# Performance work log

Measured on AMD Instinct MI355X. Metric: run time of the kernel, lower is better.

The kernel has to match this reference:

```python
import jax, jax.numpy as jnp
import numpy as np

N_NODES = 50000


def _sage_conv(x, src, dst, W_l, b_l, W_r):
    # PyG SAGEConv (aggr='mean'): out = lin_l(mean_{j in N(i)} x_j) + lin_r(x_i)
    # lin_l has bias, lin_r has no bias.
    neigh_sum = jax.ops.segment_sum(x[src], dst, num_segments=N_NODES)  # [N, F]
    deg = jax.ops.segment_sum(jnp.ones_like(dst, dtype=x.dtype), dst, num_segments=N_NODES)
    neigh_mean = neigh_sum / jnp.maximum(deg, 1.0)[:, None]
    return neigh_mean @ W_l.T + b_l + x @ W_r.T


def setup_inputs() -> dict:
    key = jax.random.key(0)
    ks = jax.random.split(key, 8)
    D, H, C = 768, 128, 4
    x = jax.random.normal(ks[0], (N_NODES, D), dtype=jnp.float32)
    edge_index = jax.random.randint(ks[1], (2, 800000), 0, N_NODES, dtype=jnp.int64)
    s1 = 1.0 / np.sqrt(D)
    s2 = 1.0 / np.sqrt(H)
    return {
        "x": x,
        "edge_index": edge_index,
        "W1_l": jax.random.uniform(ks[2], (H, D), jnp.float32, -s1, s1),
        "b1_l": jnp.zeros((H,), jnp.float32),
        "W1_r": jax.random.uniform(ks[3], (H, D), jnp.float32, -s1, s1),
        "W2_l": jax.random.uniform(ks[4], (C, H), jnp.float32, -s2, s2),
        "b2_l": jnp.zeros((C,), jnp.float32),
        "W2_r": jax.random.uniform(ks[5], (C, H), jnp.float32, -s2, s2),
    }


def reference(x, edge_index, W1_l, b1_l, W1_r, W2_l, b2_l, W2_r):
    src, dst = edge_index[0], edge_index[1]
    h = jax.nn.relu(_sage_conv(x, src, dst, W1_l, b1_l, W1_r))  # [N, H]
    out = _sage_conv(h, src, dst, W2_l, b2_l, W2_r)  # [N, C]
    return out
```

## Files before the change

### kernel.cpp

```cpp
#include <hip/hip_runtime.h>


typedef __bf16 bf16x8 __attribute__((ext_vector_type(8)));
typedef float  f32x4  __attribute__((ext_vector_type(4)));

__device__ __forceinline__ float bf16_lo(uint32_t w) {
    union { uint32_t u; float f; } c; c.u = w << 16; return c.f;
}
__device__ __forceinline__ float bf16_hi(uint32_t w) {
    union { uint32_t u; float f; } c; c.u = w & 0xffff0000u; return c.f;
}

__global__ __launch_bounds__(256)
void prep(const float* __restrict__ W1l, const float* __restrict__ W1r,
          __bf16* __restrict__ Bp, int* __restrict__ deg, int N)
{
    int i = blockIdx.x * 256 + threadIdx.x;
    if (i < N) deg[i] = 0;
    if (i < 256 * 768) {
        int col = i / 768, k = i - col * 768;
        float v = (col < 128) ? W1l[col * 768 + k] : W1r[(col - 128) * 768 + k];
        Bp[((k >> 3) << 11) + (col << 3) + (k & 7)] = (__bf16)v;
    }
}

__global__ __launch_bounds__(512)
void gemm_bf16(const float* __restrict__ A, const __bf16* __restrict__ Bp,
               __bf16* __restrict__ Cb, int M)
{
    constexpr int LDK = 72;
    __shared__ __bf16 As[64][LDK];
    const int bm   = blockIdx.x * 64;
    const int tid  = threadIdx.x;
    const int lane = tid & 63;
    const int wave = tid >> 6;
    const int wr = wave >> 2, wc = wave & 3;
    const int l15 = lane & 15;
    const int lk  = lane >> 4;

    f32x4 acc[2][4] = {};
    float4 apref[2];

    const int arow = tid >> 3;
    const int akc  = (tid & 7) << 3;
    const __bf16* bbase = Bp + ((size_t)(wc * 64 + l15) << 3) + ((size_t)lk << 11);

    auto load_A = [&](int k0) {
        if (bm + arow < M) {
            const float* src = A + (size_t)(bm + arow) * 768 + k0 + akc;
            apref[0] = *(const float4*)src;
            apref[1] = *(const float4*)(src + 4);
        } else {
            apref[0] = make_float4(0.f, 0.f, 0.f, 0.f);
            apref[1] = make_float4(0.f, 0.f, 0.f, 0.f);
        }
    };

    load_A(0);
    for (int kt = 0; kt < 12; ++kt) {
        if (kt) __syncthreads();
        {
            float4 f0 = apref[0], f1 = apref[1];
            bf16x8 b;
            b[0] = (__bf16)f0.x; b[1] = (__bf16)f0.y;
            b[2] = (__bf16)f0.z; b[3] = (__bf16)f0.w;
            b[4] = (__bf16)f1.x; b[5] = (__bf16)f1.y;
            b[6] = (__bf16)f1.z; b[7] = (__bf16)f1.w;
            *(bf16x8*)&As[arow][akc] = b;
        }
        __syncthreads();
        if (kt < 11) load_A((kt + 1) * 64);

        bf16x8 bcur[2][4];
        #pragma unroll
        for (int ks = 0; ks < 2; ++ks)
            #pragma unroll
            for (int j = 0; j < 4; ++j)
                bcur[ks][j] = *(const bf16x8*)(bbase +
                    (((size_t)(kt * 8 + ks * 4) << 11) + ((size_t)j << 7)));

        #pragma unroll
        for (int ks = 0; ks < 2; ++ks) {
            int koff = ks * 32 + lk * 8;
            bf16x8 af[2];
            #pragma unroll
            for (int i = 0; i < 2; ++i)
                af[i] = *(const bf16x8*)&As[wr * 32 + i * 16 + l15][koff];
            #pragma unroll
            for (int i = 0; i < 2; ++i)
                #pragma unroll
                for (int j = 0; j < 4; ++j)
                    acc[i][j] = __builtin_amdgcn_mfma_f32_16x16x32_bf16(
                        af[i], bcur[ks][j], acc[i][j], 0, 0, 0);
        }
    }

    #pragma unroll
    for (int i = 0; i < 2; ++i)
        #pragma unroll
        for (int j = 0; j < 4; ++j)
            #pragma unroll
            for (int v = 0; v < 4; ++v) {
                int row = bm + wr * 32 + i * 16 + lk * 4 + v;
                int col = wc * 64 + j * 16 + l15;
                if (row < M) Cb[(size_t)row * 256 + col] = (__bf16)acc[i][j][v];
            }
}

__global__ __launch_bounds__(256)
void csr_count(const int* __restrict__ ei, int* __restrict__ deg, int E)
{
    int e = blockIdx.x * 256 + threadIdx.x;
    if (e >= E) return;
    atomicAdd(&deg[ei[E + e]], 1);
}

__global__ __launch_bounds__(1024)
void scan1(const int* __restrict__ deg, int* __restrict__ row_ptr,
           int* __restrict__ partials, int N)
{
    __shared__ int buf[1024];
    int i = blockIdx.x * 1024 + threadIdx.x;
    int v = (i < N) ? deg[i] : 0;
    int val = v;
    buf[threadIdx.x] = val;
    __syncthreads();
    for (int off = 1; off < 1024; off <<= 1) {
        int t = (threadIdx.x >= (unsigned)off) ? buf[threadIdx.x - off] : 0;
        __syncthreads();
        val += t;
        buf[threadIdx.x] = val;
        __syncthreads();
    }
    if (i < N) row_ptr[i] = val - v;
    if (threadIdx.x == 1023) partials[blockIdx.x] = val;
}

__global__ __launch_bounds__(64)
void scan2(int* __restrict__ partials, int nb, int* __restrict__ row_ptr,
           int N, int E)
{
    int lane = threadIdx.x;
    int v = (lane < nb) ? partials[lane] : 0;
    int s = v;
    #pragma unroll
    for (int off = 1; off < 64; off <<= 1) {
        int t = __shfl_up(s, off);
        if (lane >= off) s += t;
    }
    if (lane < nb) partials[lane] = s - v;
    if (lane == 0) row_ptr[N] = E;
}

__global__ __launch_bounds__(1024)
void scan3(int* __restrict__ row_ptr, int* __restrict__ cursor,
           const int* __restrict__ partials, int N)
{
    int i = blockIdx.x * 1024 + threadIdx.x;
    if (i >= N) return;
    int v = row_ptr[i] + partials[blockIdx.x];
    row_ptr[i] = v;
    cursor[i]  = v;
}

__global__ __launch_bounds__(256)
void csr_fill(const int* __restrict__ ei, int* __restrict__ cursor,
              int* __restrict__ csr_src, int E)
{
    int e = blockIdx.x * 256 + threadIdx.x;
    if (e >= E) return;
    int src = ei[e];
    int dst = ei[E + e];
    int pos = atomicAdd(&cursor[dst], 1);
    csr_src[pos] = src;
}

__global__ __launch_bounds__(256)
void sage1_fused(const int* __restrict__ row_ptr, const int* __restrict__ csr_src,
                 const __bf16* __restrict__ pq, const float* __restrict__ b1,
                 const float* __restrict__ W2l, const float* __restrict__ W2r,
                 float* __restrict__ r, float* __restrict__ s, int N)
{
    __shared__ float Wl[512], Wr[512];
    for (int i = threadIdx.x; i < 512; i += 256) {
        Wl[i] = W2l[i];
        Wr[i] = W2r[i];
    }
    __syncthreads();

    int wid  = threadIdx.x >> 6;
    int lane = threadIdx.x & 63;
    int g = lane >> 3;
    int l = lane & 7;
    int n = blockIdx.x * 4 + wid;
    if (n >= N) return;
    int beg = row_ptr[n], end = row_ptr[n + 1];

    float a0[8] = {}, a1[8] = {};
    for (int eb = beg; eb < end; eb += 64) {
        int cnt = min(64, end - eb);
        int id = (eb + lane < end) ? csr_src[eb + lane] : 0;
        for (int t = 0; t < cnt; t += 8) {
            int src = __shfl(id, t + g);
            if (t + g < cnt) {
                const __bf16* row = pq + (size_t)src * 256;
                uint4 w0 = *(const uint4*)(row + l * 8);
                uint4 w1 = *(const uint4*)(row + 64 + l * 8);
                a0[0] += bf16_lo(w0.x); a0[1] += bf16_hi(w0.x);
                a0[2] += bf16_lo(w0.y); a0[3] += bf16_hi(w0.y);
                a0[4] += bf16_lo(w0.z); a0[5] += bf16_hi(w0.z);
                a0[6] += bf16_lo(w0.w); a0[7] += bf16_hi(w0.w);
                a1[0] += bf16_lo(w1.x); a1[1] += bf16_hi(w1.x);
                a1[2] += bf16_lo(w1.y); a1[3] += bf16_hi(w1.y);
                a1[4] += bf16_lo(w1.z); a1[5] += bf16_hi(w1.z);
                a1[6] += bf16_lo(w1.w); a1[7] += bf16_hi(w1.w);
            }
        }
    }
    #pragma unroll
    for (int c = 0; c < 8; ++c) {
        a0[c] += __shfl_xor(a0[c], 8);  a1[c] += __shfl_xor(a1[c], 8);
        a0[c] += __shfl_xor(a0[c], 16); a1[c] += __shfl_xor(a1[c], 16);
        a0[c] += __shfl_xor(a0[c], 32); a1[c] += __shfl_xor(a1[c], 32);
    }

    float inv = 1.0f / fmaxf((float)(end - beg), 1.0f);
    const __bf16* qrow = pq + (size_t)n * 256 + 128;
    uint4  qw0 = *(const uint4*)(qrow + l * 8);
    uint4  qw1 = *(const uint4*)(qrow + 64 + l * 8);
    float4 bv00 = *(const float4*)(b1 + l * 8);
    float4 bv01 = *(const float4*)(b1 + l * 8 + 4);
    float4 bv10 = *(const float4*)(b1 + 64 + l * 8);
    float4 bv11 = *(const float4*)(b1 + 64 + l * 8 + 4);
    float h0[8], h1[8];
    h0[0] = fmaxf(a0[0] * inv + bv00.x + bf16_lo(qw0.x), 0.f);
    h0[1] = fmaxf(a0[1] * inv + bv00.y + bf16_hi(qw0.x), 0.f);
    h0[2] = fmaxf(a0[2] * inv + bv00.z + bf16_lo(qw0.y), 0.f);
    h0[3] = fmaxf(a0[3] * inv + bv00.w + bf16_hi(qw0.y), 0.f);
    h0[4] = fmaxf(a0[4] * inv + bv01.x + bf16_lo(qw0.z), 0.f);
    h0[5] = fmaxf(a0[5] * inv + bv01.y + bf16_hi(qw0.z), 0.f);
    h0[6] = fmaxf(a0[6] * inv + bv01.z + bf16_lo(qw0.w), 0.f);
    h0[7] = fmaxf(a0[7] * inv + bv01.w + bf16_hi(qw0.w), 0.f);
    h1[0] = fmaxf(a1[0] * inv + bv10.x + bf16_lo(qw1.x), 0.f);
    h1[1] = fmaxf(a1[1] * inv + bv10.y + bf16_hi(qw1.x), 0.f);
    h1[2] = fmaxf(a1[2] * inv + bv10.z + bf16_lo(qw1.y), 0.f);
    h1[3] = fmaxf(a1[3] * inv + bv10.w + bf16_hi(qw1.y), 0.f);
    h1[4] = fmaxf(a1[4] * inv + bv11.x + bf16_lo(qw1.z), 0.f);
    h1[5] = fmaxf(a1[5] * inv + bv11.y + bf16_hi(qw1.z), 0.f);
    h1[6] = fmaxf(a1[6] * inv + bv11.z + bf16_lo(qw1.w), 0.f);
    h1[7] = fmaxf(a1[7] * inv + bv11.w + bf16_hi(qw1.w), 0.f);

    float part[8];
    #pragma unroll
    for (int c = 0; c < 4; ++c) {
        float pl = 0.f, pr = 0.f;
        #pragma unroll
        for (int j = 0; j < 8; ++j) {
            pl = fmaf(h0[j], Wl[c * 128 + l * 8 + j], pl);
            pl = fmaf(h1[j], Wl[c * 128 + 64 + l * 8 + j], pl);
            pr = fmaf(h0[j], Wr[c * 128 + l * 8 + j], pr);
            pr = fmaf(h1[j], Wr[c * 128 + 64 + l * 8 + j], pr);
        }
        part[c] = pl; part[4 + c] = pr;
    }
    #pragma unroll
    for (int off = 4; off; off >>= 1)
        #pragma unroll
        for (int c = 0; c < 8; ++c)
            part[c] += __shfl_xor(part[c], off);
    if (lane == 0) {
        *(float4*)(r + (size_t)n * 4) = make_float4(part[0], part[1], part[2], part[3]);
        *(float4*)(s + (size_t)n * 4) = make_float4(part[4], part[5], part[6], part[7]);
    }
}

__global__ __launch_bounds__(256)
void sage2_gather(const int* __restrict__ row_ptr, const int* __restrict__ csr_src,
                  const float* __restrict__ r, const float* __restrict__ s,
                  const float* __restrict__ b2, float* __restrict__ out, int N)
{
    int t = blockIdx.x * 256 + threadIdx.x;
    if (t >= N * 4) return;
    int n = t >> 2, c = t & 3;
    int beg = row_ptr[n], end = row_ptr[n + 1];
    float acc = 0.f;
    for (int e = beg; e < end; ++e)
        acc += r[(size_t)csr_src[e] * 4 + c];
    out[t] = acc / fmaxf((float)(end - beg), 1.0f) + b2[c] + s[t];
}

extern "C" void kernel_launch(void* const* d_in, const int* in_sizes, int n_in,
                              void* d_out, int out_size, void* d_ws, size_t ws_size,
                              hipStream_t stream)
{
    const float* x   = (const float*)d_in[0];
    const int*   ei  = (const int*)d_in[1];
    const float* W1l = (const float*)d_in[2];
    const float* b1l = (const float*)d_in[3];
    const float* W1r = (const float*)d_in[4];
    const float* W2l = (const float*)d_in[5];
    const float* b2l = (const float*)d_in[6];
    const float* W2r = (const float*)d_in[7];
    float* out = (float*)d_out;

    const int N = in_sizes[0] / 768;
    const int E = in_sizes[1] / 2;
    const int NB = (N + 1023) / 1024;

    char* ws = (char*)d_ws;
    size_t off = 0;
    auto alloc = [&](size_t bytes) -> void* {
        void* pp = ws + off;
        off += (bytes + 255) & ~(size_t)255;
        return pp;
    };
    __bf16* pq      = (__bf16*)alloc((size_t)N * 256 * 2);
    float*  r       = (float*)alloc((size_t)N * 4 * 4);
    float*  s       = (float*)alloc((size_t)N * 4 * 4);
    __bf16* Bp      = (__bf16*)alloc((size_t)256 * 768 * 2);
    int*    deg     = (int*)alloc((size_t)N * 4);
    int*    row_ptr = (int*)alloc((size_t)(N + 1) * 4);
    int*    cursor  = (int*)alloc((size_t)N * 4);
    int*    csr_src = (int*)alloc((size_t)E * 4);
    int*    partials= (int*)alloc((size_t)64 * 4);

    prep<<<(256 * 768 + 255) / 256, 256, 0, stream>>>(W1l, W1r, Bp, deg, N);

    gemm_bf16<<<(N + 63) / 64, 512, 0, stream>>>(x, Bp, pq, N);

    csr_count<<<(E + 255) / 256, 256, 0, stream>>>(ei, deg, E);
    scan1<<<NB, 1024, 0, stream>>>(deg, row_ptr, partials, N);
    scan2<<<1, 64, 0, stream>>>(partials, NB, row_ptr, N, E);
    scan3<<<NB, 1024, 0, stream>>>(row_ptr, cursor, partials, N);
    csr_fill<<<(E + 255) / 256, 256, 0, stream>>>(ei, cursor, csr_src, E);

    sage1_fused<<<(N + 3) / 4, 256, 0, stream>>>(row_ptr, csr_src, pq, b1l,
                                                 W2l, W2r, r, s, N);

    sage2_gather<<<(N * 4 + 255) / 256, 256, 0, stream>>>(row_ptr, csr_src, r, s, b2l, out, N);
}
```

Baseline: 221.6 us.

## Fuse CSR fill into GEMM launch, merge scan passes, widen GEMM K-tile

Scan phases 2 and 3 are merged into one kernel in which each block recomputes the partial-sum prefix itself. The CSR fill is folded into the GEMM launch as 256 extra blocks that scatter edges while the other blocks run the bf16 MFMA GEMM, so the atomic-heavy fill can overlap the compute. The GEMM K-tile is doubled from 64 to 128, giving 6 iterations instead of 12 and halving the barrier count, at the cost of more LDS and registers per block. The changes remove two launches and the serialization between GEMM and CSR construction, but the fill blocks may compete with GEMM blocks for CU slots.

```diff
diff --git a/kernel.cpp b/kernel.cpp
--- a/kernel.cpp
+++ b/kernel.cpp
@@ -22,89 +22,6 @@
         float v = (col < 128) ? W1l[col * 768 + k] : W1r[(col - 128) * 768 + k];
         Bp[((k >> 3) << 11) + (col << 3) + (k & 7)] = (__bf16)v;
     }
-}
-
-__global__ __launch_bounds__(512)
-void gemm_bf16(const float* __restrict__ A, const __bf16* __restrict__ Bp,
-               __bf16* __restrict__ Cb, int M)
-{
-    constexpr int LDK = 72;
-    __shared__ __bf16 As[64][LDK];
-    const int bm   = blockIdx.x * 64;
-    const int tid  = threadIdx.x;
-    const int lane = tid & 63;
-    const int wave = tid >> 6;
-    const int wr = wave >> 2, wc = wave & 3;
-    const int l15 = lane & 15;
-    const int lk  = lane >> 4;
-
-    f32x4 acc[2][4] = {};
-    float4 apref[2];
-
-    const int arow = tid >> 3;
-    const int akc  = (tid & 7) << 3;
-    const __bf16* bbase = Bp + ((size_t)(wc * 64 + l15) << 3) + ((size_t)lk << 11);
-
-    auto load_A = [&](int k0) {
-        if (bm + arow < M) {
-            const float* src = A + (size_t)(bm + arow) * 768 + k0 + akc;
-            apref[0] = *(const float4*)src;
-            apref[1] = *(const float4*)(src + 4);
-        } else {
-            apref[0] = make_float4(0.f, 0.f, 0.f, 0.f);
-            apref[1] = make_float4(0.f, 0.f, 0.f, 0.f);
-        }
-    };
-
-    load_A(0);
-    for (int kt = 0; kt < 12; ++kt) {
-        if (kt) __syncthreads();
-        {
-            float4 f0 = apref[0], f1 = apref[1];
-            bf16x8 b;
-            b[0] = (__bf16)f0.x; b[1] = (__bf16)f0.y;
-            b[2] = (__bf16)f0.z; b[3] = (__bf16)f0.w;
-            b[4] = (__bf16)f1.x; b[5] = (__bf16)f1.y;
-            b[6] = (__bf16)f1.z; b[7] = (__bf16)f1.w;
-            *(bf16x8*)&As[arow][akc] = b;
-        }
-        __syncthreads();
-        if (kt < 11) load_A((kt + 1) * 64);
-
-        bf16x8 bcur[2][4];
-        #pragma unroll
-        for (int ks = 0; ks < 2; ++ks)
-            #pragma unroll
-            for (int j = 0; j < 4; ++j)
-                bcur[ks][j] = *(const bf16x8*)(bbase +
-                    (((size_t)(kt * 8 + ks * 4) << 11) + ((size_t)j << 7)));
-
-        #pragma unroll
-        for (int ks = 0; ks < 2; ++ks) {
-            int koff = ks * 32 + lk * 8;
-            bf16x8 af[2];
-            #pragma unroll
-            for (int i = 0; i < 2; ++i)
-                af[i] = *(const bf16x8*)&As[wr * 32 + i * 16 + l15][koff];
-            #pragma unroll
-            for (int i = 0; i < 2; ++i)
-                #pragma unroll
-                for (int j = 0; j < 4; ++j)
-                    acc[i][j] = __builtin_amdgcn_mfma_f32_16x16x32_bf16(
-                        af[i], bcur[ks][j], acc[i][j], 0, 0, 0);
-        }
-    }
-
-    #pragma unroll
-    for (int i = 0; i < 2; ++i)
-        #pragma unroll
-        for (int j = 0; j < 4; ++j)
-            #pragma unroll
-            for (int v = 0; v < 4; ++v) {
-                int row = bm + wr * 32 + i * 16 + lk * 4 + v;
-                int col = wc * 64 + j * 16 + l15;
-                if (row < M) Cb[(size_t)row * 256 + col] = (__bf16)acc[i][j][v];
-            }
 }
 
 __global__ __launch_bounds__(256)
@@ -136,43 +53,137 @@
     if (threadIdx.x == 1023) partials[blockIdx.x] = val;
 }
 
-__global__ __launch_bounds__(64)
-void scan2(int* __restrict__ partials, int nb, int* __restrict__ row_ptr,
-           int N, int E)
-{
-    int lane = threadIdx.x;
-    int v = (lane < nb) ? partials[lane] : 0;
-    int s = v;
+__global__ __launch_bounds__(1024)
+void scan23(int* __restrict__ row_ptr, int* __restrict__ cursor,
+            const int* __restrict__ partials, int N, int E, int nb)
+{
+    __shared__ int soff;
+    int b = blockIdx.x;
+    if (threadIdx.x < 64) {
+        int lane = threadIdx.x;
+        int v = (lane < nb) ? partials[lane] : 0;
+        int s = v;
+        #pragma unroll
+        for (int off = 1; off < 64; off <<= 1) {
+            int t = __shfl_up(s, off);
+            if (lane >= off) s += t;
+        }
+        if (lane == b) soff = s - v;
+    }
+    __syncthreads();
+    int off = soff;
+    int i = b * 1024 + threadIdx.x;
+    if (i < N) {
+        int v = row_ptr[i] + off;
+        row_ptr[i] = v;
+        cursor[i]  = v;
+    }
+    if (b == 0 && threadIdx.x == 0) row_ptr[N] = E;
+}
+
+__global__ __launch_bounds__(512)
+void gemm_fill(const float* __restrict__ A, const __bf16* __restrict__ Bp,
+               __bf16* __restrict__ Cb, int M, int mtiles,
+               const int* __restrict__ ei, int* __restrict__ cursor,
+               int* __restrict__ csr_src, int E)
+{
+    constexpr int LDK = 136;
+    __shared__ __bf16 As[64][LDK];
+    const int tid = threadIdx.x;
+
+    if ((int)blockIdx.x >= mtiles) {
+        int stride = (gridDim.x - mtiles) * 512;
+        for (int e = (blockIdx.x - mtiles) * 512 + tid; e < E; e += stride) {
+            int src = ei[e];
+            int dst = ei[E + e];
+            int pos = atomicAdd(&cursor[dst], 1);
+            csr_src[pos] = src;
+        }
+        return;
+    }
+
+    const int bm   = blockIdx.x * 64;
+    const int lane = tid & 63;
+    const int wave = tid >> 6;
+    const int wr = wave >> 2, wc = wave & 3;
+    const int l15 = lane & 15;
+    const int lk  = lane >> 4;
+
+    f32x4 acc[2][4] = {};
+    float4 apref[4];
+
+    const int arow = tid >> 3;
+    const int akc  = (tid & 7) << 4;
+    const __bf16* bbase = Bp + ((size_t)(wc * 64 + l15) << 3) + ((size_t)lk << 11);
+
+    auto load_A = [&](int k0) {
+        if (bm + arow < M) {
+            const float* src = A + (size_t)(bm + arow) * 768 + k0 + akc;
+            apref[0] = *(const float4*)src;
+            apref[1] = *(const float4*)(src + 4);
+            apref[2] = *(const float4*)(src + 8);
+            apref[3] = *(const float4*)(src + 12);
+        } else {
+            apref[0] = apref[1] = apref[2] = apref[3] = make_float4(0.f, 0.f, 0.f, 0.f);
+        }
+    };
+
+    load_A(0);
+    for (int kt = 0; kt < 6; ++kt) {
+        if (kt) __syncthreads();
+        {
+            bf16x8 b0, b1;
+            b0[0] = (__bf16)apref[0].x; b0[1] = (__bf16)apref[0].y;
+            b0[2] = (__bf16)apref[0].z; b0[3] = (__bf16)apref[0].w;
+            b0[4] = (__bf16)apref[1].x; b0[5] = (__bf16)apref[1].y;
+            b0[6] = (__bf16)apref[1].z; b0[7] = (__bf16)apref[1].w;
+            b1[0] = (__bf16)apref[2].x; b1[1] = (__bf16)apref[2].y;
+            b1[2] = (__bf16)apref[2].z; b1[3] = (__bf16)apref[2].w;
+            b1[4] = (__bf16)apref[3].x; b1[5] = (__bf16)apref[3].y;
+            b1[6] = (__bf16)apref[3].z; b1[7] = (__bf16)apref[3].w;
+            *(bf16x8*)&As[arow][akc]     = b0;
+            *(bf16x8*)&As[arow][akc + 8] = b1;
+        }
+        __syncthreads();
+        if (kt < 5) load_A((kt + 1) * 128);
+
+        #pragma unroll
+        for (int ksp = 0; ksp < 2; ++ksp) {
+            bf16x8 bcur[2][4];
+            #pragma unroll
+            for (int k2 = 0; k2 < 2; ++k2)
+                #pragma unroll
+                for (int j = 0; j < 4; ++j)
+                    bcur[k2][j] = *(const bf16x8*)(bbase +
+                        (((size_t)(kt * 16 + (ksp * 2 + k2) * 4) << 11) +
+                         ((size_t)j << 7)));
+            #pragma unroll
+            for (int k2 = 0; k2 < 2; ++k2) {
+                int koff = (ksp * 2 + k2) * 32 + lk * 8;
+                bf16x8 af[2];
+                #pragma unroll
+                for (int i = 0; i < 2; ++i)
+                    af[i] = *(const bf16x8*)&As[wr * 32 + i * 16 + l15][koff];
+                #pragma unroll
+                for (int i = 0; i < 2; ++i)
+                    #pragma unroll
+                    for (int j = 0; j < 4; ++j)
+                        acc[i][j] = __builtin_amdgcn_mfma_f32_16x16x32_bf16(
+                            af[i], bcur[k2][j], acc[i][j], 0, 0, 0);
+            }
+        }
+    }
+
     #pragma unroll
-    for (int off = 1; off < 64; off <<= 1) {
-        int t = __shfl_up(s, off);
-        if (lane >= off) s += t;
-    }
-    if (lane < nb) partials[lane] = s - v;
-    if (lane == 0) row_ptr[N] = E;
-}
-
-__global__ __launch_bounds__(1024)
-void scan3(int* __restrict__ row_ptr, int* __restrict__ cursor,
-           const int* __restrict__ partials, int N)
-{
-    int i = blockIdx.x * 1024 + threadIdx.x;
-    if (i >= N) return;
-    int v = row_ptr[i] + partials[blockIdx.x];
-    row_ptr[i] = v;
-    cursor[i]  = v;
-}
-
-__global__ __launch_bounds__(256)
-void csr_fill(const int* __restrict__ ei, int* __restrict__ cursor,
-              int* __restrict__ csr_src, int E)
-{
-    int e = blockIdx.x * 256 + threadIdx.x;
-    if (e >= E) return;
-    int src = ei[e];
-    int dst = ei[E + e];
-    int pos = atomicAdd(&cursor[dst], 1);
-    csr_src[pos] = src;
+    for (int i = 0; i < 2; ++i)
+        #pragma unroll
+        for (int j = 0; j < 4; ++j)
+            #pragma unroll
+            for (int v = 0; v < 4; ++v) {
+                int row = bm + wr * 32 + i * 16 + lk * 4 + v;
+                int col = wc * 64 + j * 16 + l15;
+                if (row < M) Cb[(size_t)row * 256 + col] = (__bf16)acc[i][j][v];
+            }
 }
 
 __global__ __launch_bounds__(256)
@@ -326,13 +337,13 @@
 
     prep<<<(256 * 768 + 255) / 256, 256, 0, stream>>>(W1l, W1r, Bp, deg, N);
 
-    gemm_bf16<<<(N + 63) / 64, 512, 0, stream>>>(x, Bp, pq, N);
-
     csr_count<<<(E + 255) / 256, 256, 0, stream>>>(ei, deg, E);
     scan1<<<NB, 1024, 0, stream>>>(deg, row_ptr, partials, N);
-    scan2<<<1, 64, 0, stream>>>(partials, NB, row_ptr, N, E);
-    scan3<<<NB, 1024, 0, stream>>>(row_ptr, cursor, partials, N);
-    csr_fill<<<(E + 255) / 256, 256, 0, stream>>>(ei, cursor, csr_src, E);
+    scan23<<<NB, 1024, 0, stream>>>(row_ptr, cursor, partials, N, E, NB);
+
+    const int mtiles = (N + 63) / 64;
+    gemm_fill<<<mtiles + 256, 512, 0, stream>>>(x, Bp, pq, N, mtiles,
+                                                ei, cursor, csr_src, E);
 
     sage1_fused<<<(N + 3) / 4, 256, 0, stream>>>(row_ptr, csr_src, pq, b1l,
                                                  W2l, W2r, r, s, N);
```

After: 204.4 us. 7.8% less time.

## Fuse CSR fill into GEMM launch, merge scan passes, stage GEMM stores via LDS

Applied to the files above, without the earlier changes.

The counting pass now records each edge's slot from the atomic return value, so the fill pass no longer needs atomics or a cursor array. The fill work is appended as extra blocks of the GEMM launch so it runs alongside the GEMM, and scan2/scan3 are merged into a single kernel. GEMM output is staged through shared memory to make coalesced 16-byte stores. Together these cut two launches and the second round of atomics, at the cost of an extra E-sized slot array and more LDS per GEMM block.

```diff
diff --git a/kernel.cpp b/kernel.cpp
--- a/kernel.cpp
+++ b/kernel.cpp
@@ -24,14 +24,82 @@
     }
 }
 
+__global__ __launch_bounds__(256)
+void csr_count(const int* __restrict__ ei, int* __restrict__ deg,
+               int* __restrict__ slot, int E)
+{
+    int e = blockIdx.x * 256 + threadIdx.x;
+    if (e >= E) return;
+    slot[e] = atomicAdd(&deg[ei[E + e]], 1);
+}
+
+__global__ __launch_bounds__(1024)
+void scan1(const int* __restrict__ deg, int* __restrict__ row_ptr,
+           int* __restrict__ partials, int N)
+{
+    __shared__ int buf[1024];
+    int i = blockIdx.x * 1024 + threadIdx.x;
+    int v = (i < N) ? deg[i] : 0;
+    int val = v;
+    buf[threadIdx.x] = val;
+    __syncthreads();
+    for (int off = 1; off < 1024; off <<= 1) {
+        int t = (threadIdx.x >= (unsigned)off) ? buf[threadIdx.x - off] : 0;
+        __syncthreads();
+        val += t;
+        buf[threadIdx.x] = val;
+        __syncthreads();
+    }
+    if (i < N) row_ptr[i] = val - v;
+    if (threadIdx.x == 1023) partials[blockIdx.x] = val;
+}
+
+__global__ __launch_bounds__(1024)
+void scan23(int* __restrict__ row_ptr, const int* __restrict__ partials,
+            int N, int E, int nb)
+{
+    __shared__ int soff;
+    int b = blockIdx.x;
+    if (threadIdx.x < 64) {
+        int lane = threadIdx.x;
+        int v = (lane < nb) ? partials[lane] : 0;
+        int s = v;
+        #pragma unroll
+        for (int off = 1; off < 64; off <<= 1) {
+            int t = __shfl_up(s, off);
+            if (lane >= off) s += t;
+        }
+        if (lane == b) soff = s - v;
+    }
+    __syncthreads();
+    int off = soff;
+    int i = b * 1024 + threadIdx.x;
+    if (i < N) row_ptr[i] += off;
+    if (b == 0 && threadIdx.x == 0) row_ptr[N] = E;
+}
+
 __global__ __launch_bounds__(512)
-void gemm_bf16(const float* __restrict__ A, const __bf16* __restrict__ Bp,
-               __bf16* __restrict__ Cb, int M)
+void gemm_fill(const float* __restrict__ A, const __bf16* __restrict__ Bp,
+               __bf16* __restrict__ Cb, int M, int gblocks,
+               const int* __restrict__ ei, const int* __restrict__ row_ptr,
+               const int* __restrict__ slot, int* __restrict__ csr_src, int E)
 {
     constexpr int LDK = 72;
     __shared__ __bf16 As[64][LDK];
+    __shared__ __bf16 Cs[64][136];
+    const int tid = threadIdx.x;
+
+    if ((int)blockIdx.x >= gblocks) {
+        int e = (blockIdx.x - gblocks) * 512 + tid;
+        if (e < E) {
+            int src = ei[e];
+            int dst = ei[E + e];
+            csr_src[row_ptr[dst] + slot[e]] = src;
+        }
+        return;
+    }
+
     const int bm   = blockIdx.x * 64;
-    const int tid  = threadIdx.x;
     const int lane = tid & 63;
     const int wave = tid >> 6;
     const int wr = wave >> 2, wc = wave & 3;
@@ -96,83 +164,29 @@
     }
 
     #pragma unroll
-    for (int i = 0; i < 2; ++i)
-        #pragma unroll
-        for (int j = 0; j < 4; ++j)
+    for (int half = 0; half < 2; ++half) {
+        __syncthreads();
+        if ((wc >> 1) == half) {
+            int cb = (wc & 1) * 64;
             #pragma unroll
-            for (int v = 0; v < 4; ++v) {
-                int row = bm + wr * 32 + i * 16 + lk * 4 + v;
-                int col = wc * 64 + j * 16 + l15;
-                if (row < M) Cb[(size_t)row * 256 + col] = (__bf16)acc[i][j][v];
-            }
-}
-
-__global__ __launch_bounds__(256)
-void csr_count(const int* __restrict__ ei, int* __restrict__ deg, int E)
-{
-    int e = blockIdx.x * 256 + threadIdx.x;
-    if (e >= E) return;
-    atomicAdd(&deg[ei[E + e]], 1);
-}
-
-__global__ __launch_bounds__(1024)
-void scan1(const int* __restrict__ deg, int* __restrict__ row_ptr,
-           int* __restrict__ partials, int N)
-{
-    __shared__ int buf[1024];
-    int i = blockIdx.x * 1024 + threadIdx.x;
-    int v = (i < N) ? deg[i] : 0;
-    int val = v;
-    buf[threadIdx.x] = val;
-    __syncthreads();
-    for (int off = 1; off < 1024; off <<= 1) {
-        int t = (threadIdx.x >= (unsigned)off) ? buf[threadIdx.x - off] : 0;
-        __syncthreads();
-        val += t;
-        buf[threadIdx.x] = val;
-        __syncthreads();
-    }
-    if (i < N) row_ptr[i] = val - v;
-    if (threadIdx.x == 1023) partials[blockIdx.x] = val;
-}
-
-__global__ __launch_bounds__(64)
-void scan2(int* __restrict__ partials, int nb, int* __restrict__ row_ptr,
-           int N, int E)
-{
-    int lane = threadIdx.x;
-    int v = (lane < nb) ? partials[lane] : 0;
-    int s = v;
-    #pragma unroll
-    for (int off = 1; off < 64; off <<= 1) {
-        int t = __shfl_up(s, off);
-        if (lane >= off) s += t;
-    }
-    if (lane < nb) partials[lane] = s - v;
-    if (lane == 0) row_ptr[N] = E;
-}
-
-__global__ __launch_bounds__(1024)
-void scan3(int* __restrict__ row_ptr, int* __restrict__ cursor,
-           const int* __restrict__ partials, int N)
-{
-    int i = blockIdx.x * 1024 + threadIdx.x;
-    if (i >= N) return;
-    int v = row_ptr[i] + partials[blockIdx.x];
-    row_ptr[i] = v;
-    cursor[i]  = v;
-}
-
-__global__ __launch_bounds__(256)
-void csr_fill(const int* __restrict__ ei, int* __restrict__ cursor,
-              int* __restrict__ csr_src, int E)
-{
-    int e = blockIdx.x * 256 + threadIdx.x;
-    if (e >= E) return;
-    int src = ei[e];
-    int dst = ei[E + e];
-    int pos = atomicAdd(&cursor[dst], 1);
-    csr_src[pos] = src;
+            for (int i = 0; i < 2; ++i)
+                #pragma unroll
+                for (int j = 0; j < 4; ++j)
+                    #pragma unroll
+                    for (int v = 0; v < 4; ++v)
+                        Cs[wr * 32 + i * 16 + lk * 4 + v][cb + j * 16 + l15] =
+                            (__bf16)acc[i][j][v];
+        }
+        __syncthreads();
+        #pragma unroll
+        for (int it = 0; it < 2; ++it) {
+            int idx = it * 512 + tid;
+            int row = idx >> 4, ch = idx & 15;
+            if (bm + row < M)
+                *(bf16x8*)(Cb + (size_t)(bm + row) * 256 + half * 128 + ch * 8) =
+                    *(const bf16x8*)&Cs[row][ch * 8];
+        }
+    }
 }
 
 __global__ __launch_bounds__(256)
@@ -306,6 +320,8 @@
     const int N = in_sizes[0] / 768;
     const int E = in_sizes[1] / 2;
     const int NB = (N + 1023) / 1024;
+    const int gblocks = (N + 63) / 64;
+    const int fblocks = (E + 511) / 512;
 
     char* ws = (char*)d_ws;
     size_t off = 0;
@@ -320,19 +336,19 @@
     __bf16* Bp      = (__bf16*)alloc((size_t)256 * 768 * 2);
     int*    deg     = (int*)alloc((size_t)N * 4);
     int*    row_ptr = (int*)alloc((size_t)(N + 1) * 4);
-    int*    cursor  = (int*)alloc((size_t)N * 4);
+    int*    slot    = (int*)alloc((size_t)E * 4);
     int*    csr_src = (int*)alloc((size_t)E * 4);
     int*    partials= (int*)alloc((size_t)64 * 4);
 
     prep<<<(256 * 768 + 255) / 256, 256, 0, stream>>>(W1l, W1r, Bp, deg, N);
 
-    gemm_bf16<<<(N + 63) / 64, 512, 0, stream>>>(x, Bp, pq, N);
-
-    csr_count<<<(E + 255) / 256, 256, 0, stream>>>(ei, deg, E);
+    csr_count<<<(E + 255) / 256, 256, 0, stream>>>(ei, deg, slot, E);
     scan1<<<NB, 1024, 0, stream>>>(deg, row_ptr, partials, N);
-    scan2<<<1, 64, 0, stream>>>(partials, NB, row_ptr, N, E);
-    scan3<<<NB, 1024, 0, stream>>>(row_ptr, cursor, partials, N);
-    csr_fill<<<(E + 255) / 256, 256, 0, stream>>>(ei, cursor, csr_src, E);
+    scan23<<<NB, 1024, 0, stream>>>(row_ptr, partials, N, E, NB);
+
+    gemm_fill<<<gblocks + fblocks, 512, 0, stream>>>(x, Bp, pq, N, gblocks,
+                                                     ei, row_ptr, slot,
+                                                     csr_src, E);
 
     sage1_fused<<<(N + 3) / 4, 256, 0, stream>>>(row_ptr, csr_src, pq, b1l,
                                                  W2l, W2r, r, s, N);
```

Measured after the change: 189.5 us. -14.5%, faster.
